# Optimization experiments

Measured on AMD Instinct MI355X. Metric: run time of the kernel, lower is better.

The kernel has to match this reference:

```python
import jax, jax.numpy as jnp
import numpy as np

B, C, Dd, Hh, Ww = 2, 512, 8, 8, 16
D_STATE, D_CONV, EXPAND = 16, 4, 2
D_INNER = EXPAND * C
DT_RANK = -(-C // 16)  # ceil(C/16), Mamba default dt_rank


def setup_inputs() -> dict:
    key = jax.random.key(0)
    ks = jax.random.split(key, 8)
    s = 0.02
    return {
        "x": jax.random.normal(ks[0], (B, C, Dd, Hh, Ww), jnp.float32),
        "gamma": jnp.ones((C,), jnp.float32),
        "beta": jnp.zeros((C,), jnp.float32),
        "W_in": jax.random.normal(ks[1], (C, 2 * D_INNER), jnp.float32) * s,
        "conv_w": jax.random.normal(ks[2], (D_INNER, D_CONV), jnp.float32) * s,
        "conv_b": jnp.zeros((D_INNER,), jnp.float32),
        "W_x": jax.random.normal(ks[3], (D_INNER, DT_RANK + 2 * D_STATE), jnp.float32) * s,
        "W_dt": jax.random.normal(ks[4], (DT_RANK, D_INNER), jnp.float32) * s,
        "b_dt": jax.random.normal(ks[5], (D_INNER,), jnp.float32) * s,
        "A_log": jnp.log(jnp.broadcast_to(jnp.arange(1, D_STATE + 1, dtype=jnp.float32), (D_INNER, D_STATE))),
        "D_param": jnp.ones((D_INNER,), jnp.float32),
        "W_out": jax.random.normal(ks[6], (D_INNER, C), jnp.float32) * s,
    }


def reference(x, gamma, beta, W_in, conv_w, conv_b, W_x, W_dt, b_dt, A_log, D_param, W_out):
    b, c, d, h, w = x.shape
    L = d * h * w
    dt_rank = W_dt.shape[0]
    n = A_log.shape[1]
    kc = conv_w.shape[1]

    # (B,C,D,H,W) -> (B,L,C)
    xs = x.transpose(0, 2, 3, 4, 1).reshape(b, L, c)

    # LayerNorm over channels
    mu = xs.mean(-1, keepdims=True)
    var = ((xs - mu) ** 2).mean(-1, keepdims=True)
    xn = (xs - mu) * jax.lax.rsqrt(var + 1e-5) * gamma + beta

    # Mamba: in_proj -> (x, z)
    xz = xn @ W_in                       # (b,L,2*di)
    xi, z = jnp.split(xz, 2, axis=-1)

    # causal depthwise conv1d (kernel kc) + SiLU
    xp = jnp.pad(xi, ((0, 0), (kc - 1, 0), (0, 0)))
    xc = conv_b + sum(conv_w[:, k] * xp[:, k:k + L, :] for k in range(kc))
    xc = jax.nn.silu(xc)                 # (b,L,di)

    # x_proj -> dt, B, C (input-dependent)
    proj = xc @ W_x
    dtr = proj[..., :dt_rank]
    Bm = proj[..., dt_rank:dt_rank + n]   # (b,L,n)
    Cm = proj[..., dt_rank + n:]          # (b,L,n)
    dt = jax.nn.softplus(dtr @ W_dt + b_dt)  # (b,L,di)

    A = -jnp.exp(A_log)                  # (di,n)
    dA = jnp.exp(dt[..., None] * A)      # (b,L,di,n)
    dBx = (dt * xc)[..., None] * Bm[:, :, None, :]  # (b,L,di,n)

    def step(hc, inp):
        dA_t, dBx_t, C_t = inp
        hc = dA_t * hc + dBx_t
        return hc, jnp.einsum('bdn,bn->bd', hc, C_t)

    h0 = jnp.zeros((b, dA.shape[2], n), xc.dtype)
    _, ys = jax.lax.scan(step, h0, (dA.transpose(1, 0, 2, 3), dBx.transpose(1, 0, 2, 3), Cm.transpose(1, 0, 2)))
    y = ys.transpose(1, 0, 2) + D_param * xc   # (b,L,di)
    y = y * jax.nn.silu(z)

    out = y @ W_out                      # (b,L,c)
    out = out.reshape(b, d, h, w, c).transpose(0, 4, 1, 2, 3)
    return out + x
```

## Files before the change

### kernel.cpp

```cpp
#include <hip/hip_runtime.h>
#include <hip/hip_bf16.h>


typedef __attribute__((ext_vector_type(8))) short bf16x8;
typedef __attribute__((ext_vector_type(4))) float f32x4;

#define DEV __device__ __forceinline__

DEV short f2bf(float f) {
    union { float f; unsigned u; } v;
    v.f = f;
    unsigned r = v.u + 0x7fffu + ((v.u >> 16) & 1u);
    return (short)(r >> 16);
}
DEV float bf2f(short s) {
    union { float f; unsigned u; } v;
    v.u = ((unsigned)(unsigned short)s) << 16;
    return v.f;
}

__global__ void k_prep(const float* __restrict__ x, const float* __restrict__ Win,
                       const float* __restrict__ Wx, const float* __restrict__ Wdt,
                       const float* __restrict__ Wout, const float* __restrict__ Alog,
                       const float* __restrict__ convw,
                       short* __restrict__ WinT, short* __restrict__ WxT,
                       short* __restrict__ WdtT, short* __restrict__ WoutT,
                       float* __restrict__ xT, float* __restrict__ Aneg,
                       float* __restrict__ cwT) {
    __shared__ float T[64][65];
    int bx = blockIdx.x, tid = threadIdx.x;
    int ii = tid >> 6, jj = tid & 63;

    if (bx < 256) {
        int b = bx >> 7, rem = bx & 127, ct = rem >> 4, lt = rem & 15;
        int c0 = ct * 64, l0 = lt * 64;
        #pragma unroll
        for (int k = 0; k < 16; k++) {
            int c = ii * 16 + k;
            T[c][jj] = x[(b * 512 + c0 + c) * 1024 + l0 + jj];
        }
        __syncthreads();
        #pragma unroll
        for (int k = 0; k < 16; k++) {
            int l = ii * 16 + k;
            xT[(b * 1024 + l0 + l) * 512 + c0 + jj] = T[jj][l];
        }
        return;
    }

    auto xpose = [&](const float* src, short* dst, int R, int C, int rt, int ct) {
        int r0 = rt * 64, c0 = ct * 64;
        #pragma unroll
        for (int k = 0; k < 16; k++) {
            int r = ii * 16 + k;
            if (r0 + r < R) T[r][jj] = src[(size_t)(r0 + r) * C + c0 + jj];
        }
        __syncthreads();
        #pragma unroll
        for (int k = 0; k < 16; k++) {
            int c = ii * 16 + k;
            if (r0 + jj < R) dst[(size_t)(c0 + c) * R + r0 + jj] = f2bf(T[jj][c]);
        }
    };

    if (bx < 512)      { int i = bx - 256; xpose(Win,  WinT,  512, 2048, i >> 5, i & 31); }
    else if (bx < 640) { int i = bx - 512; xpose(Wout, WoutT, 1024, 512, i >> 3, i & 7); }
    else if (bx < 656) { int i = bx - 640; xpose(Wx,   WxT,  1024,  64, i, 0); }
    else if (bx < 672) { int i = bx - 656; xpose(Wdt,  WdtT,   32, 1024, 0, i); }
    else if (bx < 676) {
        int base = ((bx - 672) * 256 + tid) * 16;
        #pragma unroll
        for (int t = 0; t < 16; t++) Aneg[base + t] = -__expf(Alog[base + t]);
    } else {
        #pragma unroll
        for (int t = 0; t < 16; t++) {
            int idx = tid * 16 + t;
            int k = idx >> 10, d = idx & 1023;
            cwT[idx] = convw[d * 4 + k];
        }
    }
}

__global__ void k_ln(const float* __restrict__ xT, const float* __restrict__ gamma,
                     const float* __restrict__ beta, short* __restrict__ xn) {
    int tid = threadIdx.x;
    int m = blockIdx.x * 8 + (tid >> 5);
    int c0 = (tid & 31) * 16;
    float vx[16], vg[16], vb[16];
    #pragma unroll
    for (int s = 0; s < 4; s++) {
        *(float4*)&vx[s * 4] = *(const float4*)&xT[m * 512 + c0 + s * 4];
        *(float4*)&vg[s * 4] = *(const float4*)&gamma[c0 + s * 4];
        *(float4*)&vb[s * 4] = *(const float4*)&beta[c0 + s * 4];
    }
    float ps = 0.f, pq = 0.f;
    #pragma unroll
    for (int j = 0; j < 16; j++) { ps += vx[j]; pq += vx[j] * vx[j]; }
    #pragma unroll
    for (int off = 1; off < 32; off <<= 1) {
        ps += __shfl_xor(ps, off);
        pq += __shfl_xor(pq, off);
    }
    float mu = ps * (1.f / 512.f);
    float rstd = rsqrtf(pq * (1.f / 512.f) - mu * mu + 1e-5f);
    short t16[16];
    #pragma unroll
    for (int j = 0; j < 16; j++)
        t16[j] = f2bf((vx[j] - mu) * rstd * vg[j] + vb[j]);
    *(uint4*)&xn[m * 512 + c0]     = *(uint4*)&t16[0];
    *(uint4*)&xn[m * 512 + c0 + 8] = *(uint4*)&t16[8];
}

__launch_bounds__(512)
__global__ void k_gemm1(const short* __restrict__ xn, const short* __restrict__ WinT,
                        short* __restrict__ xz) {
    constexpr int LDT = 40;
    __shared__ __align__(16) short As[128 * LDT];
    __shared__ __align__(16) short Bs[128 * LDT];
    int tid = threadIdx.x, lane = tid & 63, wave = tid >> 6;
    int quad = lane >> 4, r16 = lane & 15;
    int wmi = wave >> 2, wni = wave & 3;
    int blockM = blockIdx.y * 128, blockN = blockIdx.x * 128;
    f32x4 acc[4][2] = {};

    for (int k0 = 0; k0 < 512; k0 += 32) {
        {
            int row = tid >> 2, seg = tid & 3;
            *(uint4*)&As[row * LDT + seg * 8] =
                *(const uint4*)&xn[(blockM + row) * 512 + k0 + seg * 8];
            *(uint4*)&Bs[row * LDT + seg * 8] =
                *(const uint4*)&WinT[(blockN + row) * 512 + k0 + seg * 8];
        }
        __syncthreads();
        bf16x8 af[4], bf8[2];
        #pragma unroll
        for (int i = 0; i < 4; i++)
            af[i] = *(const bf16x8*)&As[(wmi * 64 + i * 16 + r16) * LDT + quad * 8];
        #pragma unroll
        for (int j = 0; j < 2; j++)
            bf8[j] = *(const bf16x8*)&Bs[(wni * 32 + j * 16 + r16) * LDT + quad * 8];
        #pragma unroll
        for (int i = 0; i < 4; i++)
            #pragma unroll
            for (int j = 0; j < 2; j++)
                acc[i][j] = __builtin_amdgcn_mfma_f32_16x16x32_bf16(af[i], bf8[j], acc[i][j], 0, 0, 0);
        __syncthreads();
    }
    #pragma unroll
    for (int i = 0; i < 4; i++)
        #pragma unroll
        for (int j = 0; j < 2; j++)
            #pragma unroll
            for (int rr = 0; rr < 4; rr++) {
                int row = blockM + wmi * 64 + i * 16 + quad * 4 + rr;
                int col = blockN + wni * 32 + j * 16 + r16;
                xz[row * 2048 + col] = f2bf(acc[i][j][rr]);
            }
}

__launch_bounds__(256)
__global__ void k_convgemm2(const short* __restrict__ xz, const float* __restrict__ cwT,
                            const float* __restrict__ convb, const short* __restrict__ WxT,
                            short* __restrict__ xcb, float* __restrict__ projP) {
    constexpr int LDT = 140;
    __shared__ __align__(16) short As[64 * LDT];
    __shared__ __align__(16) short Bs[64 * LDT];
    int tid = threadIdx.x, lane = tid & 63, wave = tid >> 6;
    int quad = lane >> 4, r16 = lane & 15;
    int kc = blockIdx.x, mt = blockIdx.y;
    int blockM = mt * 64, d0 = kc * 128;

    #pragma unroll
    for (int g = 0; g < 4; g++) {
        int task = tid + 256 * g;
        int r = task >> 4, u = task & 15;
        int m = blockM + r, dl = u * 8, d = d0 + dl;
        float a8[8];
        {
            float4 b0 = *(const float4*)&convb[d];
            float4 b1 = *(const float4*)&convb[d + 4];
            a8[0] = b0.x; a8[1] = b0.y; a8[2] = b0.z; a8[3] = b0.w;
            a8[4] = b1.x; a8[5] = b1.y; a8[6] = b1.z; a8[7] = b1.w;
        }
        int lrow = m & 1023;
        #pragma unroll
        for (int k = 0; k < 4; k++) {
            if (lrow - 3 + k >= 0) {
                uint4 raw = *(const uint4*)&xz[(m - 3 + k) * 2048 + d];
                short* sp = (short*)&raw;
                float4 w0 = *(const float4*)&cwT[k * 1024 + d];
                float4 w1 = *(const float4*)&cwT[k * 1024 + d + 4];
                a8[0] += w0.x * bf2f(sp[0]); a8[1] += w0.y * bf2f(sp[1]);
                a8[2] += w0.z * bf2f(sp[2]); a8[3] += w0.w * bf2f(sp[3]);
                a8[4] += w1.x * bf2f(sp[4]); a8[5] += w1.y * bf2f(sp[5]);
                a8[6] += w1.z * bf2f(sp[6]); a8[7] += w1.w * bf2f(sp[7]);
            }
        }
        short t8[8];
        #pragma unroll
        for (int j = 0; j < 8; j++)
            t8[j] = f2bf(a8[j] / (1.f + __expf(-a8[j])));
        *(uint4*)&As[r * LDT + dl] = *(uint4*)t8;
        *(uint4*)&xcb[m * 1024 + d] = *(uint4*)t8;
    }
    #pragma unroll
    for (int g = 0; g < 4; g++) {
        int task = tid + 256 * g;
        int n = task >> 4, u = task & 15;
        *(uint4*)&Bs[n * LDT + u * 8] = *(const uint4*)&WxT[n * 1024 + d0 + u * 8];
    }
    __syncthreads();

    f32x4 acc[4] = {};
    #pragma unroll
    for (int ks = 0; ks < 4; ks++) {
        bf16x8 af = *(const bf16x8*)&As[(wave * 16 + r16) * LDT + ks * 32 + quad * 8];
        #pragma unroll
        for (int j = 0; j < 4; j++) {
            bf16x8 b8 = *(const bf16x8*)&Bs[(j * 16 + r16) * LDT + ks * 32 + quad * 8];
            acc[j] = __builtin_amdgcn_mfma_f32_16x16x32_bf16(af, b8, acc[j], 0, 0, 0);
        }
    }
    float* dst = projP + (size_t)kc * 131072;
    #pragma unroll
    for (int j = 0; j < 4; j++)
        #pragma unroll
        for (int rr = 0; rr < 4; rr++) {
            int row = wave * 16 + quad * 4 + rr;
            int col = j * 16 + r16;
            dst[(blockM + row) * 64 + col] = acc[j][rr];
        }
}

__launch_bounds__(256)
__global__ void k_gemm3(const float* __restrict__ projP, const short* __restrict__ WdtT,
                        const float* __restrict__ bdt, float* __restrict__ proj,
                        short* __restrict__ dth) {
    constexpr int LDT = 40;
    __shared__ __align__(16) char SMB[17408];
    short* As = (short*)SMB;
    short* Bs = (short*)(SMB + 5120);
    short* Dt = (short*)SMB;
    int tid = threadIdx.x, lane = tid & 63, wave = tid >> 6;
    int quad = lane >> 4, r16 = lane & 15;
    int wmi = wave >> 1, wni = wave & 1;
    int blockM = blockIdx.y * 64, blockN = blockIdx.x * 128;

    {
        int row = tid >> 2, seg = tid & 3;
        float s[8] = {};
        #pragma unroll
        for (int kc = 0; kc < 8; kc++) {
            const float* p = projP + (size_t)kc * 131072 + (blockM + row) * 64 + seg * 8;
            float4 a = *(const float4*)p, b = *(const float4*)(p + 4);
            s[0] += a.x; s[1] += a.y; s[2] += a.z; s[3] += a.w;
            s[4] += b.x; s[5] += b.y; s[6] += b.z; s[7] += b.w;
        }
        short t8[8];
        #pragma unroll
        for (int j = 0; j < 8; j++) t8[j] = f2bf(s[j]);
        *(uint4*)&As[row * LDT + seg * 8] = *(uint4*)t8;
    }
    #pragma unroll
    for (int idx = tid; idx < 512; idx += 256) {
        int row = idx >> 2, seg = idx & 3;
        *(uint4*)&Bs[row * LDT + seg * 8] = *(const uint4*)&WdtT[(blockN + row) * 32 + seg * 8];
    }
    if (blockIdx.x == 0) {
        int row = tid >> 2, seg = tid & 3;
        float s[8] = {};
        #pragma unroll
        for (int kc = 0; kc < 8; kc++) {
            const float* p = projP + (size_t)kc * 131072 + (blockM + row) * 64 + 32 + seg * 8;
            float4 a = *(const float4*)p, b = *(const float4*)(p + 4);
            s[0] += a.x; s[1] += a.y; s[2] += a.z; s[3] += a.w;
            s[4] += b.x; s[5] += b.y; s[6] += b.z; s[7] += b.w;
        }
        float* q = &proj[(blockM + row) * 64 + 32 + seg * 8];
        *(float4*)q = make_float4(s[0], s[1], s[2], s[3]);
        *(float4*)(q + 4) = make_float4(s[4], s[5], s[6], s[7]);
    }
    __syncthreads();

    bf16x8 af[2], b8[4];
    #pragma unroll
    for (int i = 0; i < 2; i++)
        af[i] = *(const bf16x8*)&As[(wmi * 32 + i * 16 + r16) * LDT + quad * 8];
    #pragma unroll
    for (int j = 0; j < 4; j++)
        b8[j] = *(const bf16x8*)&Bs[(wni * 64 + j * 16 + r16) * LDT + quad * 8];
    __syncthreads();

    #pragma unroll
    for (int i = 0; i < 2; i++)
        #pragma unroll
        for (int j = 0; j < 4; j++) {
            f32x4 c2 = {};
            c2 = __builtin_amdgcn_mfma_f32_16x16x32_bf16(af[i], b8[j], c2, 0, 0, 0);
            #pragma unroll
            for (int rr = 0; rr < 4; rr++) {
                int row = wmi * 32 + i * 16 + quad * 4 + rr;
                int col = wni * 64 + j * 16 + r16;
                float t = c2[rr] + bdt[blockN + col];
                float sp = (t > 20.f) ? t : __logf(1.f + __expf(t));
                Dt[row * 136 + col] = f2bf(sp);
            }
        }
    __syncthreads();
    {
        int row = tid >> 2, seg = tid & 3;
        #pragma unroll
        for (int u = 0; u < 4; u++)
            *(uint4*)&dth[(blockM + row) * 1024 + blockN + seg * 32 + u * 8] =
                *(uint4*)&Dt[row * 136 + seg * 32 + u * 8];
    }
}

__global__ void k_scanA(const short* __restrict__ dth, const short* __restrict__ xcb,
                        const float* __restrict__ proj, const float* __restrict__ Aneg,
                        float* __restrict__ segP, float* __restrict__ segQ) {
    int bx = blockIdx.x;
    int b = bx >> 7, rem = bx & 127;
    int seg = rem >> 2, dch = rem & 3;
    int tid = threadIdx.x;
    int d = dch * 256 + tid;
    int l0 = seg * 32;
    __shared__ float Bsh[32][16];
    for (int idx = tid; idx < 512; idx += 256) {
        int i = idx >> 4, n = idx & 15;
        Bsh[i][n] = proj[(b * 1024 + l0 + i) * 64 + 32 + n];
    }
    __syncthreads();
    float An[16], P[16], Q[16];
    #pragma unroll
    for (int n = 0; n < 16; n++) { An[n] = Aneg[d * 16 + n]; P[n] = 1.f; Q[n] = 0.f; }
    for (int i = 0; i < 32; i++) {
        int l = l0 + i;
        float dt = bf2f(dth[(b * 1024 + l) * 1024 + d]);
        float xc = bf2f(xcb[(b * 1024 + l) * 1024 + d]);
        float dx = dt * xc;
        #pragma unroll
        for (int n = 0; n < 16; n++) {
            float a = __expf(An[n] * dt);
            P[n] *= a;
            Q[n] = a * Q[n] + dx * Bsh[i][n];
        }
    }
    int base = ((b * 32 + seg) * 1024 + d) * 16;
    #pragma unroll
    for (int n = 0; n < 16; n++) { segP[base + n] = P[n]; segQ[base + n] = Q[n]; }
}

__global__ void k_scanB(float* __restrict__ segP, const float* __restrict__ segQ) {
    int gid = blockIdx.x * 256 + threadIdx.x;
    int b = gid >> 14, r = gid & 16383;
    float h = 0.f;
    for (int seg = 0; seg < 32; seg++) {
        int idx = (b * 32 + seg) * 16384 + r;
        float P = segP[idx], Q = segQ[idx];
        segP[idx] = h;
        h = P * h + Q;
    }
}

__global__ void k_scanC(const short* __restrict__ dth, const short* __restrict__ xcb,
                        const float* __restrict__ proj, const float* __restrict__ Aneg,
                        const float* __restrict__ segH, const short* __restrict__ xz,
                        const float* __restrict__ Dp, short* __restrict__ ybuf) {
    int bx = blockIdx.x;
    int b = bx >> 7, rem = bx & 127;
    int seg = rem >> 2, dch = rem & 3;
    int tid = threadIdx.x;
    int d = dch * 256 + tid;
    int l0 = seg * 32;
    __shared__ float Bsh[32][16], Csh[32][16];
    for (int idx = tid; idx < 512; idx += 256) {
        int i = idx >> 4, n = idx & 15;
        Bsh[i][n] = proj[(b * 1024 + l0 + i) * 64 + 32 + n];
        Csh[i][n] = proj[(b * 1024 + l0 + i) * 64 + 48 + n];
    }
    __syncthreads();
    float An[16], h[16];
    int hbase = ((b * 32 + seg) * 1024 + d) * 16;
    #pragma unroll
    for (int n = 0; n < 16; n++) { An[n] = Aneg[d * 16 + n]; h[n] = segH[hbase + n]; }
    float Dpd = Dp[d];
    for (int i = 0; i < 32; i++) {
        int l = l0 + i;
        float dt = bf2f(dth[(b * 1024 + l) * 1024 + d]);
        float xc = bf2f(xcb[(b * 1024 + l) * 1024 + d]);
        float dx = dt * xc;
        float y = 0.f;
        #pragma unroll
        for (int n = 0; n < 16; n++) {
            float a = __expf(An[n] * dt);
            h[n] = a * h[n] + dx * Bsh[i][n];
            y += h[n] * Csh[i][n];
        }
        float z = bf2f(xz[(b * 1024 + l) * 2048 + 1024 + d]);
        float sz = z / (1.f + __expf(-z));
        ybuf[(b * 1024 + l) * 1024 + d] = f2bf((y + Dpd * xc) * sz);
    }
}

__launch_bounds__(512)
__global__ void k_gemm4(const short* __restrict__ ybuf, const short* __restrict__ WoutT,
                        const float* __restrict__ x, float* __restrict__ out) {
    constexpr int LDT2 = 76;
    __shared__ __align__(16) char SMB[19456];
    short* As = (short*)SMB;
    short* Bs = (short*)(SMB + 9728);
    float (*T)[65] = (float(*)[65])SMB;
    int tid = threadIdx.x, lane = tid & 63, wave = tid >> 6;
    int quad = lane >> 4, r16 = lane & 15;
    int wmi = wave >> 2, wni = wave & 3;
    int blockM = blockIdx.y * 64, blockN = blockIdx.x * 64;
    f32x4 acc[2] = {};

    for (int k0 = 0; k0 < 1024; k0 += 64) {
        {
            int row = tid >> 3, seg = tid & 7;
            *(uint4*)&As[row * LDT2 + seg * 8] = *(const uint4*)&ybuf[(blockM + row) * 1024 + k0 + seg * 8];
            *(uint4*)&Bs[row * LDT2 + seg * 8] = *(const uint4*)&WoutT[(blockN + row) * 1024 + k0 + seg * 8];
        }
        __syncthreads();
        #pragma unroll
        for (int ks = 0; ks < 2; ks++) {
            bf16x8 af[2], b8;
            #pragma unroll
            for (int i = 0; i < 2; i++)
                af[i] = *(const bf16x8*)&As[(wmi * 32 + i * 16 + r16) * LDT2 + ks * 32 + quad * 8];
            b8 = *(const bf16x8*)&Bs[(wni * 16 + r16) * LDT2 + ks * 32 + quad * 8];
            #pragma unroll
            for (int i = 0; i < 2; i++)
                acc[i] = __builtin_amdgcn_mfma_f32_16x16x32_bf16(af[i], b8, acc[i], 0, 0, 0);
        }
        __syncthreads();
    }
    #pragma unroll
    for (int i = 0; i < 2; i++)
        #pragma unroll
        for (int rr = 0; rr < 4; rr++)
            T[wmi * 32 + i * 16 + quad * 4 + rr][wni * 16 + r16] = acc[i][rr];
    __syncthreads();
    int b = blockM >> 10, l0 = blockM & 1023;
    int ii = tid >> 6, jj = tid & 63;
    #pragma unroll
    for (int k = 0; k < 8; k++) {
        int c = ii * 8 + k;
        int gi = (b * 512 + blockN + c) * 1024 + l0 + jj;
        out[gi] = T[jj][c] + x[gi];
    }
}

extern "C" void kernel_launch(void* const* d_in, const int* in_sizes, int n_in,
                              void* d_out, int out_size, void* d_ws, size_t ws_size,
                              hipStream_t stream) {
    const float* x    = (const float*)d_in[0];
    const float* gam  = (const float*)d_in[1];
    const float* bet  = (const float*)d_in[2];
    const float* Win  = (const float*)d_in[3];
    const float* cw   = (const float*)d_in[4];
    const float* cb   = (const float*)d_in[5];
    const float* Wx   = (const float*)d_in[6];
    const float* Wdt  = (const float*)d_in[7];
    const float* bdt  = (const float*)d_in[8];
    const float* Alog = (const float*)d_in[9];
    const float* Dp   = (const float*)d_in[10];
    const float* Wout = (const float*)d_in[11];
    float* out = (float*)d_out;

    char* w = (char*)d_ws;
    size_t o = 0;
    auto alloc = [&](size_t bytes) { size_t r = o; o += (bytes + 255) & ~255ULL; return r; };

    float* projP = (float*)(w + alloc((size_t)8 * 131072 * 4));
    float* proj  = (float*)(w + alloc(131072 * 4));
    short* WinT  = (short*)(w + alloc(1048576 * 2));
    short* WxT   = (short*)(w + alloc(65536 * 2));
    short* WdtT  = (short*)(w + alloc(32768 * 2));
    short* WoutT = (short*)(w + alloc(524288 * 2));
    float* xT    = (float*)(w + alloc(1048576 * 4));
    short* xn    = (short*)(w + alloc(1048576 * 2));
    float* Aneg  = (float*)(w + alloc(16384 * 4));
    float* cwT   = (float*)(w + alloc(4096 * 4));
    short* xz    = (short*)(w + alloc((size_t)4194304 * 2));
    short* xcb   = (short*)(w + alloc(2097152 * 2));
    short* dth   = (short*)(w + alloc(2097152 * 2));
    float* segP  = (float*)(w + alloc((size_t)1048576 * 4));
    float* segQ  = (float*)(w + alloc((size_t)1048576 * 4));
    short* ybuf  = (short*)(w + alloc(2097152 * 2));
    (void)ws_size; (void)in_sizes; (void)n_in; (void)out_size;

    k_prep<<<677, 256, 0, stream>>>(x, Win, Wx, Wdt, Wout, Alog, cw,
                                    WinT, WxT, WdtT, WoutT, xT, Aneg, cwT);
    k_ln<<<256, 256, 0, stream>>>(xT, gam, bet, xn);
    k_gemm1<<<dim3(16, 16), 512, 0, stream>>>(xn, WinT, xz);
    k_convgemm2<<<dim3(8, 32), 256, 0, stream>>>(xz, cwT, cb, WxT, xcb, projP);
    k_gemm3<<<dim3(8, 32), 256, 0, stream>>>(projP, WdtT, bdt, proj, dth);
    k_scanA<<<256, 256, 0, stream>>>(dth, xcb, proj, Aneg, segP, segQ);
    k_scanB<<<128, 256, 0, stream>>>(segP, segQ);
    k_scanC<<<256, 256, 0, stream>>>(dth, xcb, proj, Aneg, segP, xz, Dp, ybuf);
    k_gemm4<<<dim3(8, 32), 512, 0, stream>>>(ybuf, WoutT, x, out);
}
```

Measured before the change: 199.6 us.

## Retile in_proj and out_proj GEMMs with register prefetch and staged stores

```diff
diff --git a/kernel.cpp b/kernel.cpp
--- a/kernel.cpp
+++ b/kernel.cpp
@@ -111,51 +111,78 @@
     *(uint4*)&xn[m * 512 + c0 + 8] = *(uint4*)&t16[8];
 }
 
-__launch_bounds__(512)
+__launch_bounds__(256)
 __global__ void k_gemm1(const short* __restrict__ xn, const short* __restrict__ WinT,
                         short* __restrict__ xz) {
-    constexpr int LDT = 40;
-    __shared__ __align__(16) short As[128 * LDT];
-    __shared__ __align__(16) short Bs[128 * LDT];
+    constexpr int LDT = 76;
+    __shared__ __align__(16) char SMB[19456 + 9728];
+    short* As = (short*)SMB;
+    short* Bs = (short*)(SMB + 19456);
+    short* Ct = (short*)SMB;
     int tid = threadIdx.x, lane = tid & 63, wave = tid >> 6;
     int quad = lane >> 4, r16 = lane & 15;
-    int wmi = wave >> 2, wni = wave & 3;
-    int blockM = blockIdx.y * 128, blockN = blockIdx.x * 128;
+    int wmi = wave >> 1, wni = wave & 1;
+    int blockM = blockIdx.y * 128, blockN = blockIdx.x * 64;
     f32x4 acc[4][2] = {};
 
-    for (int k0 = 0; k0 < 512; k0 += 32) {
-        {
-            int row = tid >> 2, seg = tid & 3;
-            *(uint4*)&As[row * LDT + seg * 8] =
-                *(const uint4*)&xn[(blockM + row) * 512 + k0 + seg * 8];
-            *(uint4*)&Bs[row * LDT + seg * 8] =
-                *(const uint4*)&WinT[(blockN + row) * 512 + k0 + seg * 8];
-        }
+    int arow = tid >> 3, aseg = tid & 7;
+    uint4 pA[4], pB[2];
+    #pragma unroll
+    for (int g = 0; g < 4; g++)
+        pA[g] = *(const uint4*)&xn[(blockM + arow + g * 32) * 512 + aseg * 8];
+    #pragma unroll
+    for (int g = 0; g < 2; g++)
+        pB[g] = *(const uint4*)&WinT[(blockN + arow + g * 32) * 512 + aseg * 8];
+
+    for (int it = 0; it < 8; it++) {
+        #pragma unroll
+        for (int g = 0; g < 4; g++)
+            *(uint4*)&As[(arow + g * 32) * LDT + aseg * 8] = pA[g];
+        #pragma unroll
+        for (int g = 0; g < 2; g++)
+            *(uint4*)&Bs[(arow + g * 32) * LDT + aseg * 8] = pB[g];
         __syncthreads();
-        bf16x8 af[4], bf8[2];
-        #pragma unroll
-        for (int i = 0; i < 4; i++)
-            af[i] = *(const bf16x8*)&As[(wmi * 64 + i * 16 + r16) * LDT + quad * 8];
+        if (it < 7) {
+            int k1 = (it + 1) * 64;
+            #pragma unroll
+            for (int g = 0; g < 4; g++)
+                pA[g] = *(const uint4*)&xn[(blockM + arow + g * 32) * 512 + k1 + aseg * 8];
+            #pragma unroll
+            for (int g = 0; g < 2; g++)
+                pB[g] = *(const uint4*)&WinT[(blockN + arow + g * 32) * 512 + k1 + aseg * 8];
+        }
+        #pragma unroll
+        for (int ks = 0; ks < 2; ks++) {
+            bf16x8 af[4], b8[2];
+            #pragma unroll
+            for (int i = 0; i < 4; i++)
+                af[i] = *(const bf16x8*)&As[(wmi * 64 + i * 16 + r16) * LDT + ks * 32 + quad * 8];
+            #pragma unroll
+            for (int j = 0; j < 2; j++)
+                b8[j] = *(const bf16x8*)&Bs[(wni * 32 + j * 16 + r16) * LDT + ks * 32 + quad * 8];
+            #pragma unroll
+            for (int i = 0; i < 4; i++)
+                #pragma unroll
+                for (int j = 0; j < 2; j++)
+                    acc[i][j] = __builtin_amdgcn_mfma_f32_16x16x32_bf16(af[i], b8[j], acc[i][j], 0, 0, 0);
+        }
+        __syncthreads();
+    }
+    #pragma unroll
+    for (int i = 0; i < 4; i++)
         #pragma unroll
         for (int j = 0; j < 2; j++)
-            bf8[j] = *(const bf16x8*)&Bs[(wni * 32 + j * 16 + r16) * LDT + quad * 8];
-        #pragma unroll
-        for (int i = 0; i < 4; i++)
-            #pragma unroll
-            for (int j = 0; j < 2; j++)
-                acc[i][j] = __builtin_amdgcn_mfma_f32_16x16x32_bf16(af[i], bf8[j], acc[i][j], 0, 0, 0);
-        __syncthreads();
-    }
-    #pragma unroll
-    for (int i = 0; i < 4; i++)
-        #pragma unroll
-        for (int j = 0; j < 2; j++)
-            #pragma unroll
-            for (int rr = 0; rr < 4; rr++) {
-                int row = blockM + wmi * 64 + i * 16 + quad * 4 + rr;
-                int col = blockN + wni * 32 + j * 16 + r16;
-                xz[row * 2048 + col] = f2bf(acc[i][j][rr]);
-            }
+            #pragma unroll
+            for (int rr = 0; rr < 4; rr++)
+                Ct[(wmi * 64 + i * 16 + quad * 4 + rr) * 68 + wni * 32 + j * 16 + r16] =
+                    f2bf(acc[i][j][rr]);
+    __syncthreads();
+    #pragma unroll
+    for (int g = 0; g < 4; g++) {
+        int row = arow + g * 32;
+        *(uint4*)&xz[(blockM + row) * 2048 + blockN + aseg * 8] =
+            *(uint4*)&Ct[row * 68 + aseg * 8];
+    }
 }
 
 __launch_bounds__(256)
@@ -403,34 +430,47 @@
     }
 }
 
-__launch_bounds__(512)
+__launch_bounds__(256)
 __global__ void k_gemm4(const short* __restrict__ ybuf, const short* __restrict__ WoutT,
                         const float* __restrict__ x, float* __restrict__ out) {
-    constexpr int LDT2 = 76;
-    __shared__ __align__(16) char SMB[19456];
+    constexpr int LDT = 76;
+    __shared__ __align__(16) char SMB[9728 + 4864];
     short* As = (short*)SMB;
     short* Bs = (short*)(SMB + 9728);
-    float (*T)[65] = (float(*)[65])SMB;
+    float (*T)[33] = (float(*)[33])SMB;
     int tid = threadIdx.x, lane = tid & 63, wave = tid >> 6;
     int quad = lane >> 4, r16 = lane & 15;
-    int wmi = wave >> 2, wni = wave & 3;
-    int blockM = blockIdx.y * 64, blockN = blockIdx.x * 64;
+    int wmi = wave >> 1, wni = wave & 1;
+    int blockM = blockIdx.y * 64, blockN = blockIdx.x * 32;
     f32x4 acc[2] = {};
 
-    for (int k0 = 0; k0 < 1024; k0 += 64) {
-        {
-            int row = tid >> 3, seg = tid & 7;
-            *(uint4*)&As[row * LDT2 + seg * 8] = *(const uint4*)&ybuf[(blockM + row) * 1024 + k0 + seg * 8];
-            *(uint4*)&Bs[row * LDT2 + seg * 8] = *(const uint4*)&WoutT[(blockN + row) * 1024 + k0 + seg * 8];
-        }
+    int arow = tid >> 3, aseg = tid & 7;
+    uint4 pA[2], pB;
+    #pragma unroll
+    for (int g = 0; g < 2; g++)
+        pA[g] = *(const uint4*)&ybuf[(blockM + arow + g * 32) * 1024 + aseg * 8];
+    pB = (arow < 32) ? *(const uint4*)&WoutT[(blockN + arow) * 1024 + aseg * 8] : make_uint4(0,0,0,0);
+
+    for (int it = 0; it < 16; it++) {
+        #pragma unroll
+        for (int g = 0; g < 2; g++)
+            *(uint4*)&As[(arow + g * 32) * LDT + aseg * 8] = pA[g];
+        if (arow < 32) *(uint4*)&Bs[arow * LDT + aseg * 8] = pB;
         __syncthreads();
+        if (it < 15) {
+            int k1 = (it + 1) * 64;
+            #pragma unroll
+            for (int g = 0; g < 2; g++)
+                pA[g] = *(const uint4*)&ybuf[(blockM + arow + g * 32) * 1024 + k1 + aseg * 8];
+            if (arow < 32) pB = *(const uint4*)&WoutT[(blockN + arow) * 1024 + k1 + aseg * 8];
+        }
         #pragma unroll
         for (int ks = 0; ks < 2; ks++) {
             bf16x8 af[2], b8;
             #pragma unroll
             for (int i = 0; i < 2; i++)
-                af[i] = *(const bf16x8*)&As[(wmi * 32 + i * 16 + r16) * LDT2 + ks * 32 + quad * 8];
-            b8 = *(const bf16x8*)&Bs[(wni * 16 + r16) * LDT2 + ks * 32 + quad * 8];
+                af[i] = *(const bf16x8*)&As[(wmi * 32 + i * 16 + r16) * LDT + ks * 32 + quad * 8];
+            b8 = *(const bf16x8*)&Bs[(wni * 16 + r16) * LDT + ks * 32 + quad * 8];
             #pragma unroll
             for (int i = 0; i < 2; i++)
                 acc[i] = __builtin_amdgcn_mfma_f32_16x16x32_bf16(af[i], b8, acc[i], 0, 0, 0);
@@ -495,11 +535,11 @@
     k_prep<<<677, 256, 0, stream>>>(x, Win, Wx, Wdt, Wout, Alog, cw,
                                     WinT, WxT, WdtT, WoutT, xT, Aneg, cwT);
     k_ln<<<256, 256, 0, stream>>>(xT, gam, bet, xn);
-    k_gemm1<<<dim3(16, 16), 512, 0, stream>>>(xn, WinT, xz);
+    k_gemm1<<<dim3(32, 16), 256, 0, stream>>>(xn, WinT, xz);
     k_convgemm2<<<dim3(8, 32), 256, 0, stream>>>(xz, cwT, cb, WxT, xcb, projP);
     k_gemm3<<<dim3(8, 32), 256, 0, stream>>>(projP, WdtT, bdt, proj, dth);
     k_scanA<<<256, 256, 0, stream>>>(dth, xcb, proj, Aneg, segP, segQ);
     k_scanB<<<128, 256, 0, stream>>>(segP, segQ);
     k_scanC<<<256, 256, 0, stream>>>(dth, xcb, proj, Aneg, segP, xz, Dp, ybuf);
-    k_gemm4<<<dim3(8, 32), 512, 0, stream>>>(ybuf, WoutT, x, out);
-}
+    k_gemm4<<<dim3(16, 32), 256, 0, stream>>>(ybuf, WoutT, x, out);
+}
```

Measured after the change: 228.8 us. +14.7%, slower.
